# Performance work log

Measured on AMD Instinct MI355X. Metric: run time of the kernel, lower is better.

Reference implementation:

```python
import jax, jax.numpy as jnp
import numpy as np

_EPS = 1e-6
_ZCA_EPS = 1e-5
NEG_SLOPE_ATTN = 0.2   # LeakyReLU inside score_mlp
NEG_SLOPE_FFN = 0.1    # VNLinearLeakyReLU negative_slope


def _safe_norm(x, axis, keepdims=False):
    # norm with zero-gradient at exactly-zero vectors (matches torch subgradient)
    sq = jnp.sum(x * x, axis=axis, keepdims=keepdims)
    safe = jnp.where(sq == 0, 1.0, sq)
    return jnp.sqrt(safe) * (sq > 0)


def vn_linear(W, x):
    # W: (out, in); x: (B, C_in, 3, N) -> (B, C_out, 3, N)
    return jnp.einsum('oi,bivn->bovn', W, x)


def zca_layernorm(x, gamma):
    # x: (B, C, 3, N); whiten the 3D vector components per batch element
    B, C = x.shape[0], x.shape[1]
    xf = x.reshape(B, C, 3, -1).transpose(0, 2, 1, 3).reshape(B, 3, -1)
    xf = xf.astype(jnp.float32)
    mu = xf.mean(axis=-1, keepdims=True)
    xc = xf - mu
    M = xc.shape[-1]
    cov = (xc @ xc.transpose(0, 2, 1)) / (float(M) + _EPS)  # (B,3,3)
    cov = cov + _ZCA_EPS * jnp.eye(3, dtype=cov.dtype)[None]
    w, V = jnp.linalg.eigh(cov)
    w = jnp.maximum(w, _ZCA_EPS)
    Wm = (V * jax.lax.rsqrt(w)[:, None, :]) @ V.transpose(0, 2, 1)  # (B,3,3)
    xw = Wm @ xc
    xw = xw.reshape(B, 3, C, -1).transpose(0, 2, 1, 3).reshape(x.shape).astype(x.dtype)
    return xw * gamma[None, :, None, None]


def cwsa_attention(x, pos, Wq, Wk, Wv, Wo, W1, b1, W2, b2):
    q = vn_linear(Wq, x)  # (B,C,3,N)
    k = vn_linear(Wk, x)
    v = vn_linear(Wv, x)
    qk = q.transpose(0, 3, 1, 2)  # (B,N,C,3)
    kk = k.transpose(0, 3, 1, 2)
    vv = v.transpose(0, 3, 1, 2)
    rel = qk[:, :, None, :, :] - kk[:, None, :, :, :]      # (B,N,N,C,3)
    rel_norm = _safe_norm(rel, axis=-1)                    # (B,N,N,C)
    rel_mean = rel_norm.mean(axis=-1, keepdims=True)       # (B,N,N,1)
    rel_pos = pos[:, :, None, :] - pos[:, None, :, :]      # (B,N,N,3)
    rel_pos_norm = _safe_norm(rel_pos, axis=-1, keepdims=True)  # (B,N,N,1)
    score_in = jnp.concatenate([rel_mean, rel_pos_norm], axis=-1)  # (B,N,N,2)
    h = jax.nn.leaky_relu(score_in @ W1.T + b1, NEG_SLOPE_ATTN)
    scores = h @ W2.T + b2                                  # (B,N,N,C)
    attn = jax.nn.softmax(scores, axis=2)                   # softmax over keys j
    out = jnp.einsum('bijk,bjkd->bikd', attn, vv)           # (B,N,C,3)
    out = out.transpose(0, 2, 3, 1)                         # (B,C,3,N)
    return vn_linear(Wo, out)


def vn_leaky_relu(p, d, ns):
    # p, d: (B, C, 3, N)
    dot = jnp.sum(p * d, axis=2, keepdims=True)
    dsq = jnp.sum(d * d, axis=2, keepdims=True)
    mask = (dot >= 0).astype(p.dtype)
    proj = p - (dot / (dsq + _EPS)) * d
    return ns * p + (1.0 - ns) * (mask * p + (1.0 - mask) * proj)


def ffn(x, Wfeat, Wdir, Wffn2):
    p = vn_linear(Wfeat, x)
    d = vn_linear(Wdir, x)
    h = vn_leaky_relu(p, d, NEG_SLOPE_FFN)
    return vn_linear(Wffn2, h)


def setup_inputs() -> dict:
    key = jax.random.key(0)
    ks = jax.random.split(key, 16)
    B, C, N = 2, 128, 256
    hidden, ratio = 64, 2
    sC = 1.0 / np.sqrt(C)
    inp = {
        'x': jax.random.normal(ks[0], (B, C, 3, N), dtype=jnp.float32),
        'pos': jax.random.normal(ks[1], (B, N, 3), dtype=jnp.float32),
        'Wq': jax.random.normal(ks[2], (C, C), dtype=jnp.float32) * sC,
        'Wk': jax.random.normal(ks[3], (C, C), dtype=jnp.float32) * sC,
        'Wv': jax.random.normal(ks[4], (C, C), dtype=jnp.float32) * sC,
        'Wo': jax.random.normal(ks[5], (C, C), dtype=jnp.float32) * sC,
        'W1': jax.random.normal(ks[6], (hidden, 2), dtype=jnp.float32) * (1.0 / np.sqrt(2.0)),
        'b1': jnp.zeros((hidden,), dtype=jnp.float32),
        'W2': jax.random.normal(ks[7], (C, hidden), dtype=jnp.float32) * (1.0 / np.sqrt(hidden)),
        'b2': jnp.zeros((C,), dtype=jnp.float32),
        'gamma1': jnp.ones((C,), dtype=jnp.float32),
        'Wfeat': jax.random.normal(ks[8], (C * ratio, C), dtype=jnp.float32) * sC,
        'Wdir': jax.random.normal(ks[9], (C * ratio, C), dtype=jnp.float32) * sC,
        'Wffn2': jax.random.normal(ks[10], (C, C * ratio), dtype=jnp.float32) * (1.0 / np.sqrt(C * ratio)),
        'gamma2': jnp.ones((C,), dtype=jnp.float32),
    }
    return inp


def reference(x, pos, Wq, Wk, Wv, Wo, W1, b1, W2, b2, gamma1, Wfeat, Wdir, Wffn2, gamma2):
    a = cwsa_attention(x, pos, Wq, Wk, Wv, Wo, W1, b1, W2, b2)
    x1 = zca_layernorm(x + a, gamma1)
    f = ffn(x1, Wfeat, Wdir, Wffn2)
    return zca_layernorm(x1 + f, gamma2)
```

## Files before the change

### kernel.cpp

```cpp
#include <hip/hip_runtime.h>
#include <math.h>

#define BB 2
#define CC 128
#define NN 256
#define HH 64
#define CHX 256
#define COLS 768
#define NEG_ATTN 0.2f
#define NEG_FFN 0.1f

typedef __attribute__((ext_vector_type(8))) short short8b;
typedef __attribute__((ext_vector_type(4))) float f32x4;

__device__ __forceinline__ unsigned bf16rne(float x) {
  unsigned u = __float_as_uint(x);
  return (u + 0x7fffu + ((u >> 16) & 1u)) >> 16;
}

__global__ __launch_bounds__(256) void k_qkv(
    const float* __restrict__ x, const float* __restrict__ Wq,
    const float* __restrict__ Wk, const float* __restrict__ Wv,
    float* __restrict__ q_t, float* __restrict__ k_nat, float* __restrict__ v_t3)
{
  const int ct = blockIdx.x, which = blockIdx.y, b = blockIdx.z;
  const int col0 = ct * 16;
  __shared__ float xt[CC][16];
  const float* xb = x + (size_t)b * CC * COLS;
  for (int idx = threadIdx.x; idx < CC * 16; idx += 256) {
    int r = idx >> 4, cc = idx & 15;
    xt[r][cc] = xb[r * COLS + col0 + cc];
  }
  __syncthreads();
  const float* W = (which == 0) ? Wq : ((which == 1) ? Wk : Wv);
  const int co = threadIdx.x >> 1;
  const int cc0 = (threadIdx.x & 1) * 8;
  float acc[8];
#pragma unroll
  for (int k = 0; k < 8; k++) acc[k] = 0.f;
  const float* wrow = W + co * CC;
  for (int ci = 0; ci < CC; ci++) {
    float wv = wrow[ci];
#pragma unroll
    for (int k = 0; k < 8; k++) acc[k] = fmaf(wv, xt[ci][cc0 + k], acc[k]);
  }
#pragma unroll
  for (int k = 0; k < 8; k++) {
    int col = col0 + cc0 + k;
    int v = col >> 8, n = col & 255;
    float val = acc[k];
    if (which == 0)      q_t[((size_t)(b * NN + n) * CC + co) * 3 + v] = val;
    else if (which == 1) k_nat[(size_t)(b * CC + co) * COLS + col] = val;
    else                 v_t3[((size_t)(b * NN + n) * CC + co) * 3 + v] = val;
  }
}

__global__ __launch_bounds__(256) void k_rel(
    const float* __restrict__ q_t, const float* __restrict__ k_nat,
    const float* __restrict__ pos, float* __restrict__ rm_all,
    float* __restrict__ rp_all)
{
  const int i = blockIdx.x, b = blockIdx.y;
  const int t = threadIdx.x;
  __shared__ float qv[CC * 3];
  for (int idx = t; idx < CC * 3; idx += 256)
    qv[idx] = q_t[(size_t)(b * NN + i) * CC * 3 + idx];
  __syncthreads();
  const int j = t;
  const float* kb = k_nat + (size_t)b * CC * COLS;
  float p0 = 0.f, p1 = 0.f, p2 = 0.f, p3 = 0.f;
  for (int c = 0; c < CC; c += 4) {
    float kx0 = kb[(c + 0) * COLS + j], ky0 = kb[(c + 0) * COLS + 256 + j], kz0 = kb[(c + 0) * COLS + 512 + j];
    float kx1 = kb[(c + 1) * COLS + j], ky1 = kb[(c + 1) * COLS + 256 + j], kz1 = kb[(c + 1) * COLS + 512 + j];
    float kx2 = kb[(c + 2) * COLS + j], ky2 = kb[(c + 2) * COLS + 256 + j], kz2 = kb[(c + 2) * COLS + 512 + j];
    float kx3 = kb[(c + 3) * COLS + j], ky3 = kb[(c + 3) * COLS + 256 + j], kz3 = kb[(c + 3) * COLS + 512 + j];
    float dx, dy, dz, sq;
    dx = kx0 - qv[(c + 0) * 3]; dy = ky0 - qv[(c + 0) * 3 + 1]; dz = kz0 - qv[(c + 0) * 3 + 2];
    sq = dx * dx + dy * dy + dz * dz; p0 += (sq > 0.f) ? sqrtf(sq) : 0.f;
    dx = kx1 - qv[(c + 1) * 3]; dy = ky1 - qv[(c + 1) * 3 + 1]; dz = kz1 - qv[(c + 1) * 3 + 2];
    sq = dx * dx + dy * dy + dz * dz; p1 += (sq > 0.f) ? sqrtf(sq) : 0.f;
    dx = kx2 - qv[(c + 2) * 3]; dy = ky2 - qv[(c + 2) * 3 + 1]; dz = kz2 - qv[(c + 2) * 3 + 2];
    sq = dx * dx + dy * dy + dz * dz; p2 += (sq > 0.f) ? sqrtf(sq) : 0.f;
    dx = kx3 - qv[(c + 3) * 3]; dy = ky3 - qv[(c + 3) * 3 + 1]; dz = kz3 - qv[(c + 3) * 3 + 2];
    sq = dx * dx + dy * dy + dz * dz; p3 += (sq > 0.f) ? sqrtf(sq) : 0.f;
  }
  rm_all[(size_t)(b * NN + i) * NN + j] = ((p0 + p1) + (p2 + p3)) * (1.f / 128.f);
  float dx = pos[(b * NN + i) * 3 + 0] - pos[(b * NN + j) * 3 + 0];
  float dy = pos[(b * NN + i) * 3 + 1] - pos[(b * NN + j) * 3 + 1];
  float dz = pos[(b * NN + i) * 3 + 2] - pos[(b * NN + j) * 3 + 2];
  float sq = dx * dx + dy * dy + dz * dz;
  rp_all[(size_t)(b * NN + i) * NN + j] = (sq > 0.f) ? sqrtf(sq) : 0.f;
}

__global__ __launch_bounds__(256, 4) void k_attn(
    const float* __restrict__ rm_all, const float* __restrict__ rp_all,
    const float* __restrict__ v_t3, const float* __restrict__ W1,
    const float* __restrict__ b1, const float* __restrict__ W2,
    float* __restrict__ a_nat)
{
  const int i = blockIdx.x, chalf = blockIdx.y, b = blockIdx.z;
  const int t = threadIdx.x;
  __shared__ __align__(16) short hh_s[64 * 64];
  __shared__ __align__(16) short w2_s[64 * 64];
  __shared__ float sc_s[64 * 65];
  __shared__ float rm_s[NN], rp_s[NN];

  rm_s[t] = rm_all[(size_t)(b * NN + i) * NN + t];
  rp_s[t] = rp_all[(size_t)(b * NN + i) * NN + t];
  {
    const int cl = t >> 2, h0 = (t & 3) * 16;
    const float* wrow = W2 + (size_t)(chalf * 64 + cl) * HH + h0;
#pragma unroll
    for (int e = 0; e < 8; e++) {
      unsigned lo = bf16rne(wrow[2 * e]);
      unsigned hi = bf16rne(wrow[2 * e + 1]);
      int didx = (cl * 32 + (h0 >> 1) + e) ^ ((cl & 7) << 2);
      ((unsigned*)w2_s)[didx] = lo | (hi << 16);
    }
  }
  const int h2 = (t & 31) * 2, jgrp = t >> 5;
  const float4 w1v = *reinterpret_cast<const float4*>(W1 + 2 * h2);
  const float c0 = b1[h2], c1 = b1[h2 + 1];
  __syncthreads();

  auto phase2 = [&](int q) {
#pragma unroll
    for (int jj = 0; jj < 8; jj++) {
      int jl = jgrp * 8 + jj;
      int jg = q * 64 + jl;
      float rmv = rm_s[jg], rpv = rp_s[jg];
      float g0 = fmaf(w1v.x, rmv, fmaf(w1v.y, rpv, c0));
      float g1 = fmaf(w1v.z, rmv, fmaf(w1v.w, rpv, c1));
      g0 = (g0 >= 0.f) ? g0 : NEG_ATTN * g0;
      g1 = (g1 >= 0.f) ? g1 : NEG_ATTN * g1;
      int didx = (jl * 32 + (h2 >> 1)) ^ ((jl & 7) << 2);
      ((unsigned*)hh_s)[didx] = bf16rne(g0) | (bf16rne(g1) << 16);
    }
  };

  phase2(0);
  __syncthreads();

  const int lane = t & 63, wv = t >> 6;
  const int g8 = (lane >> 4) * 8;
  const int cdx = wv * 16 + (lane & 15);
  const short8b bfr0 = *reinterpret_cast<const short8b*>(&w2_s[(cdx * 64 + g8) ^ ((cdx & 7) << 3)]);
  const short8b bfr1 = *reinterpret_cast<const short8b*>(&w2_s[(cdx * 64 + 32 + g8) ^ ((cdx & 7) << 3)]);

  const int cl = lane;
  const int par = wv;
  const int vc = chalf * 64 + cl;
  float l = 0.f, a0 = 0.f, a1 = 0.f, a2 = 0.f;

  for (int q = 0; q < 4; q++) {
#pragma unroll
    for (int jt = 0; jt < 4; jt++) {
      int jr = jt * 16 + (lane & 15);
      short8b af0 = *reinterpret_cast<const short8b*>(&hh_s[(jr * 64 + g8) ^ ((jr & 7) << 3)]);
      short8b af1 = *reinterpret_cast<const short8b*>(&hh_s[(jr * 64 + 32 + g8) ^ ((jr & 7) << 3)]);
      f32x4 acc = {0.f, 0.f, 0.f, 0.f};
      acc = __builtin_amdgcn_mfma_f32_16x16x32_bf16(af0, bfr0, acc, 0, 0, 0);
      acc = __builtin_amdgcn_mfma_f32_16x16x32_bf16(af1, bfr1, acc, 0, 0, 0);
      int row0 = jt * 16 + (lane >> 4) * 4;
      int ccol = wv * 16 + (lane & 15);
#pragma unroll
      for (int r = 0; r < 4; r++) sc_s[(row0 + r) * 65 + ccol] = acc[r];
    }
    __syncthreads();
#pragma unroll 4
    for (int jj = 0; jj < 16; jj++) {
      int jl = jj * 4 + par;
      int jg = q * 64 + jl;
      float s = sc_s[jl * 65 + cl];
      const float* vb = v_t3 + ((size_t)(b * NN + jg) * CC + vc) * 3;
      float v0 = vb[0], v1 = vb[1], v2 = vb[2];
      float p = __expf(s);
      l += p;
      a0 = fmaf(p, v0, a0);
      a1 = fmaf(p, v1, a1);
      a2 = fmaf(p, v2, a2);
    }
    if (q < 3) phase2(q + 1);
    __syncthreads();
  }

  float* mrg = sc_s;
  if (par != 0) {
    float* mp = mrg + (cl * 3 + (par - 1)) * 4;
    mp[0] = l; mp[1] = a0; mp[2] = a1; mp[3] = a2;
  }
  __syncthreads();
  if (par == 0) {
    float L = l, A0 = a0, A1 = a1, A2 = a2;
#pragma unroll
    for (int q = 0; q < 3; q++) {
      const float* mp = mrg + (cl * 3 + q) * 4;
      L += mp[0]; A0 += mp[1]; A1 += mp[2]; A2 += mp[3];
    }
    float inv = 1.f / L;
    float* ap = a_nat + (size_t)(b * CC + vc) * COLS + i;
    ap[0] = A0 * inv; ap[256] = A1 * inv; ap[512] = A2 * inv;
  }
}

__global__ __launch_bounds__(256) void k_wo_res(
    const float* __restrict__ a_nat, const float* __restrict__ Wo,
    const float* __restrict__ x, float* __restrict__ y1)
{
  const int ct = blockIdx.x, cohalf = blockIdx.y, b = blockIdx.z;
  const int col0 = ct * 16;
  __shared__ float at[CC][16];
  const float* ab = a_nat + (size_t)b * CC * COLS;
  for (int idx = threadIdx.x; idx < CC * 16; idx += 256) {
    int r = idx >> 4, cc = idx & 15;
    at[r][cc] = ab[r * COLS + col0 + cc];
  }
  __syncthreads();
  const int co = cohalf * 64 + (threadIdx.x >> 2);
  const int cc0 = (threadIdx.x & 3) * 4;
  float acc[4];
#pragma unroll
  for (int k = 0; k < 4; k++) acc[k] = 0.f;
  const float* wrow = Wo + co * CC;
  for (int ci = 0; ci < CC; ci++) {
    float wv = wrow[ci];
#pragma unroll
    for (int k = 0; k < 4; k++) acc[k] = fmaf(wv, at[ci][cc0 + k], acc[k]);
  }
  const size_t base = (size_t)(b * CC + co) * COLS + col0 + cc0;
#pragma unroll
  for (int k = 0; k < 4; k++) y1[base + k] = x[base + k] + acc[k];
}

__global__ __launch_bounds__(1024) void k_stats(
    const float* __restrict__ y, float* __restrict__ stats)
{
  const int b = blockIdx.x;
  const float* yb = y + (size_t)b * CC * COLS;
  const int t = threadIdx.x;
  float v9[9];
#pragma unroll
  for (int k = 0; k < 9; k++) v9[k] = 0.f;
  for (int e = 0; e < 32; e++) {
    int idx = e * 1024 + t;
    int cidx = idx >> 8, n = idx & 255;
    const float* row = yb + cidx * COLS + n;
    float v0 = row[0], v1 = row[256], v2 = row[512];
    v9[0] += v0; v9[1] += v1; v9[2] += v2;
    v9[3] += v0 * v0; v9[4] += v0 * v1; v9[5] += v0 * v2;
    v9[6] += v1 * v1; v9[7] += v1 * v2; v9[8] += v2 * v2;
  }
#pragma unroll
  for (int off = 32; off >= 1; off >>= 1)
#pragma unroll
    for (int k = 0; k < 9; k++) v9[k] += __shfl_down(v9[k], off);
  __shared__ float red[16][9];
  const int wid = t >> 6, lane = t & 63;
  if (lane == 0)
#pragma unroll
    for (int k = 0; k < 9; k++) red[wid][k] = v9[k];
  __syncthreads();
  if (t == 0) {
    float tot[9];
#pragma unroll
    for (int k = 0; k < 9; k++) tot[k] = 0.f;
    for (int w = 0; w < 16; w++)
#pragma unroll
      for (int k = 0; k < 9; k++) tot[k] += red[w][k];
    const float M = (float)(CC * NN);
    float mu0 = tot[0] / M, mu1 = tot[1] / M, mu2 = tot[2] / M;
    float A[3][3];
    A[0][0] = (tot[3] - M * mu0 * mu0) / M + 1e-5f;
    A[0][1] = A[1][0] = (tot[4] - M * mu0 * mu1) / M;
    A[0][2] = A[2][0] = (tot[5] - M * mu0 * mu2) / M;
    A[1][1] = (tot[6] - M * mu1 * mu1) / M + 1e-5f;
    A[1][2] = A[2][1] = (tot[7] - M * mu1 * mu2) / M;
    A[2][2] = (tot[8] - M * mu2 * mu2) / M + 1e-5f;
    float V[3][3] = {{1.f, 0.f, 0.f}, {0.f, 1.f, 0.f}, {0.f, 0.f, 1.f}};
    for (int sweep = 0; sweep < 10; sweep++) {
      for (int pi = 0; pi < 3; pi++) {
        const int p = (pi == 2) ? 1 : 0;
        const int q = (pi == 0) ? 1 : 2;
        float apq = A[p][q];
        if (fabsf(apq) < 1e-30f) continue;
        float theta = (A[q][q] - A[p][p]) / (2.f * apq);
        float tt = 1.f / (fabsf(theta) + sqrtf(theta * theta + 1.f));
        if (theta < 0.f) tt = -tt;
        float cr = 1.f / sqrtf(tt * tt + 1.f);
        float sr = tt * cr;
        float app = A[p][p], aqq = A[q][q];
        A[p][p] = app - tt * apq;
        A[q][q] = aqq + tt * apq;
        A[p][q] = A[q][p] = 0.f;
        const int r = 3 - p - q;
        float arp = A[r][p], arq = A[r][q];
        A[r][p] = A[p][r] = cr * arp - sr * arq;
        A[r][q] = A[q][r] = sr * arp + cr * arq;
        for (int rr = 0; rr < 3; rr++) {
          float vrp = V[rr][p], vrq = V[rr][q];
          V[rr][p] = cr * vrp - sr * vrq;
          V[rr][q] = sr * vrp + cr * vrq;
        }
      }
    }
    float rs[3];
#pragma unroll
    for (int k = 0; k < 3; k++) rs[k] = rsqrtf(fmaxf(A[k][k], 1e-5f));
    float* st = stats + b * 12;
    st[0] = mu0; st[1] = mu1; st[2] = mu2;
    for (int u = 0; u < 3; u++)
      for (int v = 0; v < 3; v++) {
        float acc = 0.f;
        for (int k = 0; k < 3; k++) acc += V[u][k] * rs[k] * V[v][k];
        st[3 + u * 3 + v] = acc;
      }
  }
}

__global__ __launch_bounds__(256) void k_ffn1(
    const float* __restrict__ y1, const float* __restrict__ stats,
    const float* __restrict__ gamma, const float* __restrict__ Wfeat,
    const float* __restrict__ Wdir, float* __restrict__ hout)
{
  const int nt = blockIdx.x, cs = blockIdx.y, b = blockIdx.z;
  const int n0 = nt * 16, co0 = cs * 64;
  __shared__ float xt[CC][48];
  const float* yb = y1 + (size_t)b * CC * COLS;
  const float* st = stats + b * 12;
  for (int idx = threadIdx.x; idx < CC * 16; idx += 256) {
    int ci = idx >> 4, nn = idx & 15;
    const float* row = yb + ci * COLS + n0 + nn;
    float d0 = row[0] - st[0], d1 = row[256] - st[1], d2 = row[512] - st[2];
    float g = gamma[ci];
    xt[ci][nn]      = g * (st[3] * d0 + st[4] * d1 + st[5] * d2);
    xt[ci][16 + nn] = g * (st[6] * d0 + st[7] * d1 + st[8] * d2);
    xt[ci][32 + nn] = g * (st[9] * d0 + st[10] * d1 + st[11] * d2);
  }
  __syncthreads();
  const int co = co0 + (threadIdx.x & 63);
  const int nn0 = (threadIdx.x >> 6) * 4;
  float p[3][4], d[3][4];
#pragma unroll
  for (int v = 0; v < 3; v++)
#pragma unroll
    for (int k = 0; k < 4; k++) { p[v][k] = 0.f; d[v][k] = 0.f; }
  const float* wf = Wfeat + co * CC;
  const float* wd = Wdir + co * CC;
  for (int ci = 0; ci < CC; ci++) {
    float a = wf[ci], bb = wd[ci];
#pragma unroll
    for (int v = 0; v < 3; v++)
#pragma unroll
      for (int k = 0; k < 4; k++) {
        float xv = xt[ci][v * 16 + nn0 + k];
        p[v][k] = fmaf(a, xv, p[v][k]);
        d[v][k] = fmaf(bb, xv, d[v][k]);
      }
  }
  float* hb = hout + (size_t)(b * CHX + co) * COLS;
#pragma unroll
  for (int k = 0; k < 4; k++) {
    float dot = p[0][k] * d[0][k] + p[1][k] * d[1][k] + p[2][k] * d[2][k];
    float dsq = d[0][k] * d[0][k] + d[1][k] * d[1][k] + d[2][k] * d[2][k];
    float coef = (dot >= 0.f) ? 0.f : (1.f - NEG_FFN) * dot / (dsq + 1e-6f);
#pragma unroll
    for (int v = 0; v < 3; v++)
      hb[v * 256 + n0 + nn0 + k] = p[v][k] - coef * d[v][k];
  }
}

__global__ __launch_bounds__(256) void k_ffn2(
    const float* __restrict__ h, const float* __restrict__ Wffn2,
    const float* __restrict__ y1, const float* __restrict__ stats,
    const float* __restrict__ gamma, float* __restrict__ x2)
{
  const int ct = blockIdx.x, cohalf = blockIdx.y, b = blockIdx.z;
  const int col0 = ct * 16;
  __shared__ float ht[CHX][16];
  const float* hb = h + (size_t)b * CHX * COLS;
  for (int idx = threadIdx.x; idx < CHX * 16; idx += 256) {
    int r = idx >> 4, cc = idx & 15;
    ht[r][cc] = hb[r * COLS + col0 + cc];
  }
  __syncthreads();
  const int co = cohalf * 64 + (threadIdx.x >> 2);
  const int cc0 = (threadIdx.x & 3) * 4;
  float acc[4];
#pragma unroll
  for (int k = 0; k < 4; k++) acc[k] = 0.f;
  const float* w = Wffn2 + co * CHX;
  for (int ci = 0; ci < CHX; ci++) {
    float wv = w[ci];
#pragma unroll
    for (int k = 0; k < 4; k++) acc[k] = fmaf(wv, ht[ci][cc0 + k], acc[k]);
  }
  const int col_base = col0 + cc0;
  const int v = col_base >> 8, n = col_base & 255;
  const float* st = stats + b * 12;
  const float* yb = y1 + (size_t)(b * CC + co) * COLS + n;
  const float g = gamma[co];
  const float w0 = st[3 + v * 3 + 0], w1 = st[3 + v * 3 + 1], w2 = st[3 + v * 3 + 2];
  const size_t base = (size_t)(b * CC + co) * COLS + col_base;
#pragma unroll
  for (int k = 0; k < 4; k++) {
    float d0 = yb[k] - st[0], d1 = yb[256 + k] - st[1], d2 = yb[512 + k] - st[2];
    float xw = g * (w0 * d0 + w1 * d1 + w2 * d2);
    x2[base + k] = xw + acc[k];
  }
}

__global__ __launch_bounds__(256) void k_zca_apply(
    const float* __restrict__ y, const float* __restrict__ stats,
    const float* __restrict__ gamma, float* __restrict__ out)
{
  int idx = blockIdx.x * blockDim.x + threadIdx.x;
  int b = idx >> 15, rem = idx & 32767;
  int cidx = rem >> 8, n = rem & 255;
  const float* st = stats + b * 12;
  const size_t base = (size_t)(b * CC + cidx) * COLS + n;
  float v0 = y[base] - st[0];
  float v1 = y[base + 256] - st[1];
  float v2 = y[base + 512] - st[2];
  float g = gamma[cidx];
  out[base]       = g * (st[3] * v0 + st[4] * v1 + st[5] * v2);
  out[base + 256] = g * (st[6] * v0 + st[7] * v1 + st[8] * v2);
  out[base + 512] = g * (st[9] * v0 + st[10] * v1 + st[11] * v2);
}

extern "C" void kernel_launch(void* const* d_in, const int* in_sizes, int n_in,
                              void* d_out, int out_size, void* d_ws, size_t ws_size,
                              hipStream_t stream)
{
  (void)in_sizes; (void)n_in; (void)out_size; (void)ws_size;
  const float* x      = (const float*)d_in[0];
  const float* pos    = (const float*)d_in[1];
  const float* Wq     = (const float*)d_in[2];
  const float* Wk     = (const float*)d_in[3];
  const float* Wv     = (const float*)d_in[4];
  const float* Wo     = (const float*)d_in[5];
  const float* W1     = (const float*)d_in[6];
  const float* b1     = (const float*)d_in[7];
  const float* W2     = (const float*)d_in[8];
  const float* gamma1 = (const float*)d_in[10];
  const float* Wfeat  = (const float*)d_in[11];
  const float* Wdir   = (const float*)d_in[12];
  const float* Wffn2  = (const float*)d_in[13];
  const float* gamma2 = (const float*)d_in[14];

  float* ws = (float*)d_ws;
  const size_t QKV = (size_t)BB * NN * CC * 3;
  const size_t RM  = (size_t)BB * NN * NN;
  const size_t HB  = (size_t)BB * CHX * COLS;

  float* q_t    = ws;
  float* k_nat  = q_t    + QKV;
  float* v_t3   = k_nat  + QKV;
  float* rm_all = v_t3   + QKV;
  float* rp_all = rm_all + RM;
  float* a_nat  = rp_all + RM;
  float* y1     = a_nat  + QKV;
  float* hbuf   = y1     + QKV;
  float* x2     = hbuf   + HB;
  float* stats1 = x2     + QKV;
  float* stats2 = stats1 + 64;

  k_qkv<<<dim3(48, 3, BB), 256, 0, stream>>>(x, Wq, Wk, Wv, q_t, k_nat, v_t3);
  k_rel<<<dim3(NN, BB), 256, 0, stream>>>(q_t, k_nat, pos, rm_all, rp_all);
  k_attn<<<dim3(NN, 2, BB), 256, 0, stream>>>(rm_all, rp_all, v_t3, W1, b1, W2, a_nat);
  k_wo_res<<<dim3(48, 2, BB), 256, 0, stream>>>(a_nat, Wo, x, y1);
  k_stats<<<BB, 1024, 0, stream>>>(y1, stats1);
  k_ffn1<<<dim3(16, 4, BB), 256, 0, stream>>>(y1, stats1, gamma1, Wfeat, Wdir, hbuf);
  k_ffn2<<<dim3(48, 2, BB), 256, 0, stream>>>(hbuf, Wffn2, y1, stats1, gamma1, x2);
  k_stats<<<BB, 1024, 0, stream>>>(x2, stats2);
  k_zca_apply<<<256, 256, 0, stream>>>(x2, stats2, gamma2, (float*)d_out);
}
```

Measured before the change: 106.6 us.

## Fuse post-attention stages into two persistent kernels with grid barriers

Replaces the six launches after attention (Wo+residual, stats, ffn1, ffn2, stats, apply) with two 192-block kernels that use atomic-counter grid barriers between phases. The ZCA statistics reduction is now spread over 128 blocks writing partial sums, followed by a single-thread finalize, instead of one 1024-thread block per batch. The aim is to cut launch gaps and the serial stats kernel, at the cost of spin-wait barriers that rely on all 192 blocks being co-resident, plus an extra memset.

```diff
diff --git a/kernel.cpp b/kernel.cpp
--- a/kernel.cpp
+++ b/kernel.cpp
@@ -9,6 +9,7 @@
 #define COLS 768
 #define NEG_ATTN 0.2f
 #define NEG_FFN 0.1f
+#define NBLK 192
 
 typedef __attribute__((ext_vector_type(8))) short short8b;
 typedef __attribute__((ext_vector_type(4))) float f32x4;
@@ -16,6 +17,72 @@
 __device__ __forceinline__ unsigned bf16rne(float x) {
   unsigned u = __float_as_uint(x);
   return (u + 0x7fffu + ((u >> 16) & 1u)) >> 16;
+}
+
+__device__ __forceinline__ void grid_bar(unsigned* cnt, unsigned target) {
+  __syncthreads();
+  if (threadIdx.x == 0) {
+    __threadfence();
+    atomicAdd(cnt, 1u);
+    while (atomicAdd(cnt, 0u) < target) __builtin_amdgcn_s_sleep(8);
+    __threadfence();
+  }
+  __syncthreads();
+}
+
+__device__ void zca_fin_dev(const float* part, float* st) {
+  float tot[9];
+#pragma unroll
+  for (int k = 0; k < 9; k++) tot[k] = 0.f;
+  for (int p = 0; p < 64; p++)
+#pragma unroll
+    for (int k = 0; k < 9; k++) tot[k] += part[p * 9 + k];
+  const float M = (float)(CC * NN);
+  float mu0 = tot[0] / M, mu1 = tot[1] / M, mu2 = tot[2] / M;
+  float A[3][3];
+  A[0][0] = (tot[3] - M * mu0 * mu0) / M + 1e-5f;
+  A[0][1] = A[1][0] = (tot[4] - M * mu0 * mu1) / M;
+  A[0][2] = A[2][0] = (tot[5] - M * mu0 * mu2) / M;
+  A[1][1] = (tot[6] - M * mu1 * mu1) / M + 1e-5f;
+  A[1][2] = A[2][1] = (tot[7] - M * mu1 * mu2) / M;
+  A[2][2] = (tot[8] - M * mu2 * mu2) / M + 1e-5f;
+  float V[3][3] = {{1.f, 0.f, 0.f}, {0.f, 1.f, 0.f}, {0.f, 0.f, 1.f}};
+  for (int sweep = 0; sweep < 10; sweep++) {
+    for (int pi = 0; pi < 3; pi++) {
+      const int p = (pi == 2) ? 1 : 0;
+      const int q = (pi == 0) ? 1 : 2;
+      float apq = A[p][q];
+      if (fabsf(apq) < 1e-30f) continue;
+      float theta = (A[q][q] - A[p][p]) / (2.f * apq);
+      float tt = 1.f / (fabsf(theta) + sqrtf(theta * theta + 1.f));
+      if (theta < 0.f) tt = -tt;
+      float cr = 1.f / sqrtf(tt * tt + 1.f);
+      float sr = tt * cr;
+      float app = A[p][p], aqq = A[q][q];
+      A[p][p] = app - tt * apq;
+      A[q][q] = aqq + tt * apq;
+      A[p][q] = A[q][p] = 0.f;
+      const int r = 3 - p - q;
+      float arp = A[r][p], arq = A[r][q];
+      A[r][p] = A[p][r] = cr * arp - sr * arq;
+      A[r][q] = A[q][r] = sr * arp + cr * arq;
+      for (int rr = 0; rr < 3; rr++) {
+        float vrp = V[rr][p], vrq = V[rr][q];
+        V[rr][p] = cr * vrp - sr * vrq;
+        V[rr][q] = sr * vrp + cr * vrq;
+      }
+    }
+  }
+  float rs[3];
+#pragma unroll
+  for (int k = 0; k < 3; k++) rs[k] = rsqrtf(fmaxf(A[k][k], 1e-5f));
+  st[0] = mu0; st[1] = mu1; st[2] = mu2;
+  for (int u = 0; u < 3; u++)
+    for (int v = 0; v < 3; v++) {
+      float acc = 0.f;
+      for (int k = 0; k < 3; k++) acc += V[u][k] * rs[k] * V[v][k];
+      st[3 + u * 3 + v] = acc;
+    }
 }
 
 __global__ __launch_bounds__(256) void k_qkv(
@@ -203,228 +270,235 @@
   }
 }
 
-__global__ __launch_bounds__(256) void k_wo_res(
+__global__ __launch_bounds__(256) void k_mid(
     const float* __restrict__ a_nat, const float* __restrict__ Wo,
-    const float* __restrict__ x, float* __restrict__ y1)
+    const float* __restrict__ x, const float* __restrict__ gamma1,
+    const float* __restrict__ Wfeat, const float* __restrict__ Wdir,
+    float* __restrict__ y1, float* __restrict__ part,
+    float* __restrict__ stats, float* __restrict__ hout,
+    unsigned* __restrict__ cnt)
 {
-  const int ct = blockIdx.x, cohalf = blockIdx.y, b = blockIdx.z;
-  const int col0 = ct * 16;
-  __shared__ float at[CC][16];
-  const float* ab = a_nat + (size_t)b * CC * COLS;
-  for (int idx = threadIdx.x; idx < CC * 16; idx += 256) {
-    int r = idx >> 4, cc = idx & 15;
-    at[r][cc] = ab[r * COLS + col0 + cc];
-  }
-  __syncthreads();
-  const int co = cohalf * 64 + (threadIdx.x >> 2);
-  const int cc0 = (threadIdx.x & 3) * 4;
-  float acc[4];
-#pragma unroll
-  for (int k = 0; k < 4; k++) acc[k] = 0.f;
-  const float* wrow = Wo + co * CC;
-  for (int ci = 0; ci < CC; ci++) {
-    float wv = wrow[ci];
-#pragma unroll
-    for (int k = 0; k < 4; k++) acc[k] = fmaf(wv, at[ci][cc0 + k], acc[k]);
-  }
-  const size_t base = (size_t)(b * CC + co) * COLS + col0 + cc0;
-#pragma unroll
-  for (int k = 0; k < 4; k++) y1[base + k] = x[base + k] + acc[k];
-}
-
-__global__ __launch_bounds__(1024) void k_stats(
-    const float* __restrict__ y, float* __restrict__ stats)
+  const int g = blockIdx.x, t = threadIdx.x;
+  __shared__ __align__(16) float smem[128 * 48];
+
+  {
+    const int ct = g % 48, cohalf = (g / 48) & 1, b = g / 96;
+    const int col0 = ct * 16;
+    float* at = smem;
+    const float* ab = a_nat + (size_t)b * CC * COLS;
+    for (int idx = t; idx < CC * 16; idx += 256) {
+      int r = idx >> 4, cc = idx & 15;
+      at[r * 16 + cc] = ab[r * COLS + col0 + cc];
+    }
+    __syncthreads();
+    const int co = cohalf * 64 + (t >> 2);
+    const int cc0 = (t & 3) * 4;
+    float acc[4] = {0.f, 0.f, 0.f, 0.f};
+    const float* wrow = Wo + co * CC;
+    for (int ci = 0; ci < CC; ci++) {
+      float wv = wrow[ci];
+#pragma unroll
+      for (int k = 0; k < 4; k++) acc[k] = fmaf(wv, at[ci * 16 + cc0 + k], acc[k]);
+    }
+    const size_t base = (size_t)(b * CC + co) * COLS + col0 + cc0;
+#pragma unroll
+    for (int k = 0; k < 4; k++) y1[base + k] = x[base + k] + acc[k];
+  }
+
+  grid_bar(cnt, NBLK);
+
+  if (g < 128) {
+    const int b = g >> 6, slice = g & 63;
+    const float* yb = y1 + (size_t)b * CC * COLS;
+    float v9[9];
+#pragma unroll
+    for (int k = 0; k < 9; k++) v9[k] = 0.f;
+#pragma unroll
+    for (int e = 0; e < 2; e++) {
+      int idx = slice * 512 + e * 256 + t;
+      int cidx = idx >> 8, n = idx & 255;
+      const float* row = yb + cidx * COLS + n;
+      float v0 = row[0], v1 = row[256], v2 = row[512];
+      v9[0] += v0; v9[1] += v1; v9[2] += v2;
+      v9[3] += v0 * v0; v9[4] += v0 * v1; v9[5] += v0 * v2;
+      v9[6] += v1 * v1; v9[7] += v1 * v2; v9[8] += v2 * v2;
+    }
+#pragma unroll
+    for (int off = 32; off >= 1; off >>= 1)
+#pragma unroll
+      for (int k = 0; k < 9; k++) v9[k] += __shfl_down(v9[k], off);
+    float* red = smem;
+    const int wid = t >> 6, lane = t & 63;
+    if (lane == 0)
+#pragma unroll
+      for (int k = 0; k < 9; k++) red[wid * 9 + k] = v9[k];
+    __syncthreads();
+    if (t == 0)
+#pragma unroll
+      for (int k = 0; k < 9; k++)
+        part[(size_t)(b * 64 + slice) * 9 + k] =
+            (red[k] + red[9 + k]) + (red[18 + k] + red[27 + k]);
+  }
+
+  grid_bar(cnt, 2 * NBLK);
+
+  if (g == 0 && t == 0) {
+    zca_fin_dev(part, stats);
+    zca_fin_dev(part + 64 * 9, stats + 12);
+  }
+
+  grid_bar(cnt, 3 * NBLK);
+
+  if (g < 128) {
+    const int nt = g & 15, cs = (g >> 4) & 3, b = g >> 6;
+    const int n0 = nt * 16, co0 = cs * 64;
+    float* xt = smem;
+    const float* yb = y1 + (size_t)b * CC * COLS;
+    const float* st = stats + b * 12;
+    for (int idx = t; idx < CC * 16; idx += 256) {
+      int ci = idx >> 4, nn = idx & 15;
+      const float* row = yb + ci * COLS + n0 + nn;
+      float d0 = row[0] - st[0], d1 = row[256] - st[1], d2 = row[512] - st[2];
+      float gm = gamma1[ci];
+      xt[ci * 48 + nn]      = gm * (st[3] * d0 + st[4] * d1 + st[5] * d2);
+      xt[ci * 48 + 16 + nn] = gm * (st[6] * d0 + st[7] * d1 + st[8] * d2);
+      xt[ci * 48 + 32 + nn] = gm * (st[9] * d0 + st[10] * d1 + st[11] * d2);
+    }
+    __syncthreads();
+    const int co = co0 + (t & 63);
+    const int nn0 = (t >> 6) * 4;
+    float p[3][4], d[3][4];
+#pragma unroll
+    for (int v = 0; v < 3; v++)
+#pragma unroll
+      for (int k = 0; k < 4; k++) { p[v][k] = 0.f; d[v][k] = 0.f; }
+    const float* wf = Wfeat + co * CC;
+    const float* wd = Wdir + co * CC;
+    for (int ci = 0; ci < CC; ci++) {
+      float a = wf[ci], bb = wd[ci];
+#pragma unroll
+      for (int v = 0; v < 3; v++)
+#pragma unroll
+        for (int k = 0; k < 4; k++) {
+          float xv = xt[ci * 48 + v * 16 + nn0 + k];
+          p[v][k] = fmaf(a, xv, p[v][k]);
+          d[v][k] = fmaf(bb, xv, d[v][k]);
+        }
+    }
+    float* hb = hout + (size_t)(b * CHX + co) * COLS;
+#pragma unroll
+    for (int k = 0; k < 4; k++) {
+      float dot = p[0][k] * d[0][k] + p[1][k] * d[1][k] + p[2][k] * d[2][k];
+      float dsq = d[0][k] * d[0][k] + d[1][k] * d[1][k] + d[2][k] * d[2][k];
+      float coef = (dot >= 0.f) ? 0.f : (1.f - NEG_FFN) * dot / (dsq + 1e-6f);
+#pragma unroll
+      for (int v = 0; v < 3; v++)
+        hb[v * 256 + n0 + nn0 + k] = p[v][k] - coef * d[v][k];
+    }
+  }
+}
+
+__global__ __launch_bounds__(256) void k_tail(
+    const float* __restrict__ h, const float* __restrict__ Wffn2,
+    const float* __restrict__ y1, const float* __restrict__ stats1,
+    const float* __restrict__ gamma1, const float* __restrict__ gamma2,
+    float* __restrict__ x2, float* __restrict__ part,
+    float* __restrict__ stats2, float* __restrict__ out,
+    unsigned* __restrict__ cnt)
 {
-  const int b = blockIdx.x;
-  const float* yb = y + (size_t)b * CC * COLS;
-  const int t = threadIdx.x;
-  float v9[9];
-#pragma unroll
-  for (int k = 0; k < 9; k++) v9[k] = 0.f;
-  for (int e = 0; e < 32; e++) {
-    int idx = e * 1024 + t;
-    int cidx = idx >> 8, n = idx & 255;
-    const float* row = yb + cidx * COLS + n;
-    float v0 = row[0], v1 = row[256], v2 = row[512];
-    v9[0] += v0; v9[1] += v1; v9[2] += v2;
-    v9[3] += v0 * v0; v9[4] += v0 * v1; v9[5] += v0 * v2;
-    v9[6] += v1 * v1; v9[7] += v1 * v2; v9[8] += v2 * v2;
-  }
-#pragma unroll
-  for (int off = 32; off >= 1; off >>= 1)
-#pragma unroll
-    for (int k = 0; k < 9; k++) v9[k] += __shfl_down(v9[k], off);
-  __shared__ float red[16][9];
-  const int wid = t >> 6, lane = t & 63;
-  if (lane == 0)
-#pragma unroll
-    for (int k = 0; k < 9; k++) red[wid][k] = v9[k];
-  __syncthreads();
-  if (t == 0) {
-    float tot[9];
-#pragma unroll
-    for (int k = 0; k < 9; k++) tot[k] = 0.f;
-    for (int w = 0; w < 16; w++)
-#pragma unroll
-      for (int k = 0; k < 9; k++) tot[k] += red[w][k];
-    const float M = (float)(CC * NN);
-    float mu0 = tot[0] / M, mu1 = tot[1] / M, mu2 = tot[2] / M;
-    float A[3][3];
-    A[0][0] = (tot[3] - M * mu0 * mu0) / M + 1e-5f;
-    A[0][1] = A[1][0] = (tot[4] - M * mu0 * mu1) / M;
-    A[0][2] = A[2][0] = (tot[5] - M * mu0 * mu2) / M;
-    A[1][1] = (tot[6] - M * mu1 * mu1) / M + 1e-5f;
-    A[1][2] = A[2][1] = (tot[7] - M * mu1 * mu2) / M;
-    A[2][2] = (tot[8] - M * mu2 * mu2) / M + 1e-5f;
-    float V[3][3] = {{1.f, 0.f, 0.f}, {0.f, 1.f, 0.f}, {0.f, 0.f, 1.f}};
-    for (int sweep = 0; sweep < 10; sweep++) {
-      for (int pi = 0; pi < 3; pi++) {
-        const int p = (pi == 2) ? 1 : 0;
-        const int q = (pi == 0) ? 1 : 2;
-        float apq = A[p][q];
-        if (fabsf(apq) < 1e-30f) continue;
-        float theta = (A[q][q] - A[p][p]) / (2.f * apq);
-        float tt = 1.f / (fabsf(theta) + sqrtf(theta * theta + 1.f));
-        if (theta < 0.f) tt = -tt;
-        float cr = 1.f / sqrtf(tt * tt + 1.f);
-        float sr = tt * cr;
-        float app = A[p][p], aqq = A[q][q];
-        A[p][p] = app - tt * apq;
-        A[q][q] = aqq + tt * apq;
-        A[p][q] = A[q][p] = 0.f;
-        const int r = 3 - p - q;
-        float arp = A[r][p], arq = A[r][q];
-        A[r][p] = A[p][r] = cr * arp - sr * arq;
-        A[r][q] = A[q][r] = sr * arp + cr * arq;
-        for (int rr = 0; rr < 3; rr++) {
-          float vrp = V[rr][p], vrq = V[rr][q];
-          V[rr][p] = cr * vrp - sr * vrq;
-          V[rr][q] = sr * vrp + cr * vrq;
-        }
-      }
-    }
-    float rs[3];
-#pragma unroll
-    for (int k = 0; k < 3; k++) rs[k] = rsqrtf(fmaxf(A[k][k], 1e-5f));
-    float* st = stats + b * 12;
-    st[0] = mu0; st[1] = mu1; st[2] = mu2;
-    for (int u = 0; u < 3; u++)
-      for (int v = 0; v < 3; v++) {
-        float acc = 0.f;
-        for (int k = 0; k < 3; k++) acc += V[u][k] * rs[k] * V[v][k];
-        st[3 + u * 3 + v] = acc;
-      }
-  }
-}
-
-__global__ __launch_bounds__(256) void k_ffn1(
-    const float* __restrict__ y1, const float* __restrict__ stats,
-    const float* __restrict__ gamma, const float* __restrict__ Wfeat,
-    const float* __restrict__ Wdir, float* __restrict__ hout)
-{
-  const int nt = blockIdx.x, cs = blockIdx.y, b = blockIdx.z;
-  const int n0 = nt * 16, co0 = cs * 64;
-  __shared__ float xt[CC][48];
-  const float* yb = y1 + (size_t)b * CC * COLS;
-  const float* st = stats + b * 12;
-  for (int idx = threadIdx.x; idx < CC * 16; idx += 256) {
-    int ci = idx >> 4, nn = idx & 15;
-    const float* row = yb + ci * COLS + n0 + nn;
-    float d0 = row[0] - st[0], d1 = row[256] - st[1], d2 = row[512] - st[2];
-    float g = gamma[ci];
-    xt[ci][nn]      = g * (st[3] * d0 + st[4] * d1 + st[5] * d2);
-    xt[ci][16 + nn] = g * (st[6] * d0 + st[7] * d1 + st[8] * d2);
-    xt[ci][32 + nn] = g * (st[9] * d0 + st[10] * d1 + st[11] * d2);
-  }
-  __syncthreads();
-  const int co = co0 + (threadIdx.x & 63);
-  const int nn0 = (threadIdx.x >> 6) * 4;
-  float p[3][4], d[3][4];
-#pragma unroll
-  for (int v = 0; v < 3; v++)
-#pragma unroll
-    for (int k = 0; k < 4; k++) { p[v][k] = 0.f; d[v][k] = 0.f; }
-  const float* wf = Wfeat + co * CC;
-  const float* wd = Wdir + co * CC;
-  for (int ci = 0; ci < CC; ci++) {
-    float a = wf[ci], bb = wd[ci];
-#pragma unroll
-    for (int v = 0; v < 3; v++)
-#pragma unroll
-      for (int k = 0; k < 4; k++) {
-        float xv = xt[ci][v * 16 + nn0 + k];
-        p[v][k] = fmaf(a, xv, p[v][k]);
-        d[v][k] = fmaf(bb, xv, d[v][k]);
-      }
-  }
-  float* hb = hout + (size_t)(b * CHX + co) * COLS;
-#pragma unroll
-  for (int k = 0; k < 4; k++) {
-    float dot = p[0][k] * d[0][k] + p[1][k] * d[1][k] + p[2][k] * d[2][k];
-    float dsq = d[0][k] * d[0][k] + d[1][k] * d[1][k] + d[2][k] * d[2][k];
-    float coef = (dot >= 0.f) ? 0.f : (1.f - NEG_FFN) * dot / (dsq + 1e-6f);
-#pragma unroll
-    for (int v = 0; v < 3; v++)
-      hb[v * 256 + n0 + nn0 + k] = p[v][k] - coef * d[v][k];
-  }
-}
-
-__global__ __launch_bounds__(256) void k_ffn2(
-    const float* __restrict__ h, const float* __restrict__ Wffn2,
-    const float* __restrict__ y1, const float* __restrict__ stats,
-    const float* __restrict__ gamma, float* __restrict__ x2)
-{
-  const int ct = blockIdx.x, cohalf = blockIdx.y, b = blockIdx.z;
-  const int col0 = ct * 16;
-  __shared__ float ht[CHX][16];
-  const float* hb = h + (size_t)b * CHX * COLS;
-  for (int idx = threadIdx.x; idx < CHX * 16; idx += 256) {
-    int r = idx >> 4, cc = idx & 15;
-    ht[r][cc] = hb[r * COLS + col0 + cc];
-  }
-  __syncthreads();
-  const int co = cohalf * 64 + (threadIdx.x >> 2);
-  const int cc0 = (threadIdx.x & 3) * 4;
-  float acc[4];
-#pragma unroll
-  for (int k = 0; k < 4; k++) acc[k] = 0.f;
-  const float* w = Wffn2 + co * CHX;
-  for (int ci = 0; ci < CHX; ci++) {
-    float wv = w[ci];
-#pragma unroll
-    for (int k = 0; k < 4; k++) acc[k] = fmaf(wv, ht[ci][cc0 + k], acc[k]);
-  }
-  const int col_base = col0 + cc0;
-  const int v = col_base >> 8, n = col_base & 255;
-  const float* st = stats + b * 12;
-  const float* yb = y1 + (size_t)(b * CC + co) * COLS + n;
-  const float g = gamma[co];
-  const float w0 = st[3 + v * 3 + 0], w1 = st[3 + v * 3 + 1], w2 = st[3 + v * 3 + 2];
-  const size_t base = (size_t)(b * CC + co) * COLS + col_base;
-#pragma unroll
-  for (int k = 0; k < 4; k++) {
-    float d0 = yb[k] - st[0], d1 = yb[256 + k] - st[1], d2 = yb[512 + k] - st[2];
-    float xw = g * (w0 * d0 + w1 * d1 + w2 * d2);
-    x2[base + k] = xw + acc[k];
-  }
-}
-
-__global__ __launch_bounds__(256) void k_zca_apply(
-    const float* __restrict__ y, const float* __restrict__ stats,
-    const float* __restrict__ gamma, float* __restrict__ out)
-{
-  int idx = blockIdx.x * blockDim.x + threadIdx.x;
-  int b = idx >> 15, rem = idx & 32767;
-  int cidx = rem >> 8, n = rem & 255;
-  const float* st = stats + b * 12;
-  const size_t base = (size_t)(b * CC + cidx) * COLS + n;
-  float v0 = y[base] - st[0];
-  float v1 = y[base + 256] - st[1];
-  float v2 = y[base + 512] - st[2];
-  float g = gamma[cidx];
-  out[base]       = g * (st[3] * v0 + st[4] * v1 + st[5] * v2);
-  out[base + 256] = g * (st[6] * v0 + st[7] * v1 + st[8] * v2);
-  out[base + 512] = g * (st[9] * v0 + st[10] * v1 + st[11] * v2);
+  const int g = blockIdx.x, t = threadIdx.x;
+  __shared__ __align__(16) float smem[256 * 16];
+
+  {
+    const int ct = g % 48, cohalf = (g / 48) & 1, b = g / 96;
+    const int col0 = ct * 16;
+    float* ht = smem;
+    const float* hb = h + (size_t)b * CHX * COLS;
+    for (int idx = t; idx < CHX * 16; idx += 256) {
+      int r = idx >> 4, cc = idx & 15;
+      ht[r * 16 + cc] = hb[r * COLS + col0 + cc];
+    }
+    __syncthreads();
+    const int co = cohalf * 64 + (t >> 2);
+    const int cc0 = (t & 3) * 4;
+    float acc[4] = {0.f, 0.f, 0.f, 0.f};
+    const float* w = Wffn2 + co * CHX;
+    for (int ci = 0; ci < CHX; ci++) {
+      float wv = w[ci];
+#pragma unroll
+      for (int k = 0; k < 4; k++) acc[k] = fmaf(wv, ht[ci * 16 + cc0 + k], acc[k]);
+    }
+    const int col_base = col0 + cc0;
+    const int v = col_base >> 8, n = col_base & 255;
+    const float* st = stats1 + b * 12;
+    const float* yb = y1 + (size_t)(b * CC + co) * COLS + n;
+    const float gm = gamma1[co];
+    const float w0 = st[3 + v * 3 + 0], w1 = st[3 + v * 3 + 1], w2 = st[3 + v * 3 + 2];
+    const size_t base = (size_t)(b * CC + co) * COLS + col_base;
+#pragma unroll
+    for (int k = 0; k < 4; k++) {
+      float d0 = yb[k] - st[0], d1 = yb[256 + k] - st[1], d2 = yb[512 + k] - st[2];
+      x2[base + k] = gm * (w0 * d0 + w1 * d1 + w2 * d2) + acc[k];
+    }
+  }
+
+  grid_bar(cnt, NBLK);
+
+  if (g < 128) {
+    const int b = g >> 6, slice = g & 63;
+    const float* yb = x2 + (size_t)b * CC * COLS;
+    float v9[9];
+#pragma unroll
+    for (int k = 0; k < 9; k++) v9[k] = 0.f;
+#pragma unroll
+    for (int e = 0; e < 2; e++) {
+      int idx = slice * 512 + e * 256 + t;
+      int cidx = idx >> 8, n = idx & 255;
+      const float* row = yb + cidx * COLS + n;
+      float v0 = row[0], v1 = row[256], v2 = row[512];
+      v9[0] += v0; v9[1] += v1; v9[2] += v2;
+      v9[3] += v0 * v0; v9[4] += v0 * v1; v9[5] += v0 * v2;
+      v9[6] += v1 * v1; v9[7] += v1 * v2; v9[8] += v2 * v2;
+    }
+#pragma unroll
+    for (int off = 32; off >= 1; off >>= 1)
+#pragma unroll
+      for (int k = 0; k < 9; k++) v9[k] += __shfl_down(v9[k], off);
+    float* red = smem;
+    const int wid = t >> 6, lane = t & 63;
+    if (lane == 0)
+#pragma unroll
+      for (int k = 0; k < 9; k++) red[wid * 9 + k] = v9[k];
+    __syncthreads();
+    if (t == 0)
+#pragma unroll
+      for (int k = 0; k < 9; k++)
+        part[(size_t)(b * 64 + slice) * 9 + k] =
+            (red[k] + red[9 + k]) + (red[18 + k] + red[27 + k]);
+  }
+
+  grid_bar(cnt, 2 * NBLK);
+
+  if (g == 0 && t == 0) {
+    zca_fin_dev(part, stats2);
+    zca_fin_dev(part + 64 * 9, stats2 + 12);
+  }
+
+  grid_bar(cnt, 3 * NBLK);
+
+  for (int u = g * 256 + t; u < BB * CC * NN; u += NBLK * 256) {
+    int b = u >> 15, rem = u & 32767;
+    int cidx = rem >> 8, n = rem & 255;
+    const float* st = stats2 + b * 12;
+    const size_t base = (size_t)(b * CC + cidx) * COLS + n;
+    float v0 = x2[base] - st[0];
+    float v1 = x2[base + 256] - st[1];
+    float v2 = x2[base + 512] - st[2];
+    float gm = gamma2[cidx];
+    out[base]       = gm * (st[3] * v0 + st[4] * v1 + st[5] * v2);
+    out[base + 256] = gm * (st[6] * v0 + st[7] * v1 + st[8] * v2);
+    out[base + 512] = gm * (st[9] * v0 + st[10] * v1 + st[11] * v2);
+  }
 }
 
 extern "C" void kernel_launch(void* const* d_in, const int* in_sizes, int n_in,
@@ -463,14 +537,16 @@
   float* x2     = hbuf   + HB;
   float* stats1 = x2     + QKV;
   float* stats2 = stats1 + 64;
+  float* part   = stats2 + 64;
+  unsigned* cnts = (unsigned*)(part + 1280);
+
+  hipMemsetAsync(cnts, 0, 2 * sizeof(unsigned), stream);
 
   k_qkv<<<dim3(48, 3, BB), 256, 0, stream>>>(x, Wq, Wk, Wv, q_t, k_nat, v_t3);
   k_rel<<<dim3(NN, BB), 256, 0, stream>>>(q_t, k_nat, pos, rm_all, rp_all);
   k_attn<<<dim3(NN, 2, BB), 256, 0, stream>>>(rm_all, rp_all, v_t3, W1, b1, W2, a_nat);
-  k_wo_res<<<dim3(48, 2, BB), 256, 0, stream>>>(a_nat, Wo, x, y1);
-  k_stats<<<BB, 1024, 0, stream>>>(y1, stats1);
-  k_ffn1<<<dim3(16, 4, BB), 256, 0, stream>>>(y1, stats1, gamma1, Wfeat, Wdir, hbuf);
-  k_ffn2<<<dim3(48, 2, BB), 256, 0, stream>>>(hbuf, Wffn2, y1, stats1, gamma1, x2);
-  k_stats<<<BB, 1024, 0, stream>>>(x2, stats2);
-  k_zca_apply<<<256, 256, 0, stream>>>(x2, stats2, gamma2, (float*)d_out);
-}
+  k_mid<<<NBLK, 256, 0, stream>>>(a_nat, Wo, x, gamma1, Wfeat, Wdir,
+                                  y1, part, stats1, hbuf, cnts + 0);
+  k_tail<<<NBLK, 256, 0, stream>>>(hbuf, Wffn2, y1, stats1, gamma1, gamma2,
+                                   x2, part, stats2, (float*)d_out, cnts + 1);
+}
```

Measured after the change: 183.9 us. 1.73x slower.
